# Optimization experiments

Hardware: AMD Instinct MI355X
Metric: run time of the kernel (lower is better)

The kernel has to match this reference:

```python
import jax, jax.numpy as jnp
import numpy as np

B, T, C = 512, 256, 384   # batch, seq (== block_size), n_embd
HS, BS = 64, 256          # head_size, block_size


def setup_inputs() -> dict:
    key = jax.random.key(0)
    ks = jax.random.split(key, 6)
    s = 1.0 / np.sqrt(C)
    s2 = 1.0 / np.sqrt(HS)
    return {
        "x": jax.random.normal(ks[0], (B, T, C), jnp.float32),
        "W_q": jax.random.normal(ks[1], (C, HS), jnp.float32) * s,
        "W_k": jax.random.normal(ks[2], (C, HS), jnp.float32) * s,
        "W_v": jax.random.normal(ks[3], (C, HS), jnp.float32) * s,
        "W_ql": jax.random.normal(ks[4], (HS, BS), jnp.float32) * s2,
        "W_kl": jax.random.normal(ks[5], (HS, BS), jnp.float32) * s2,
    }


def reference(x, W_q, W_k, W_v, W_ql, W_kl):
    # One head of self-attention, additive (tanh) score variant, eval mode.
    # x: [B,T,C]
    q = jnp.einsum("btc,ch->bth", x, W_q)          # [B,T,HS]
    k = jnp.einsum("btc,ch->bth", x, W_k)          # [B,T,HS]
    q_w = jnp.einsum("bth,hs->bts", q, W_ql)       # [B,T,BS]
    k_w = jnp.einsum("bth,hs->bts", k, W_kl)       # [B,T,BS]
    # NOTE: elementwise add (both [B,T,BS]) as in the torch code, then tanh.
    wei = jnp.tanh(q_w + k_w)                      # [B,T,T] since T == BS
    Tn = x.shape[1]
    causal = jnp.tril(jnp.ones((Tn, Tn), dtype=bool))
    wei = jnp.where(causal, wei, -jnp.inf)
    wei = jax.nn.softmax(wei, axis=-1)
    v = jnp.einsum("btc,ch->bth", x, W_v)          # [B,T,HS]
    out = jnp.einsum("bts,bsh->bth", wei, v)       # [B,T,HS]
    return out
```

## Files before the change

### kernel.cpp

```cpp
#include <hip/hip_runtime.h>

#define BATCH 512
#define TT    256
#define CC    384
#define HH    64

typedef float  f32x4 __attribute__((ext_vector_type(4)));
typedef short  s16x8 __attribute__((ext_vector_type(8)));

#define XS_OFF   0
#define WS_OFF   32768
#define VB_OFF   114688
#define SCR_OFF  147456
#define LDS_TOTAL 155648

__device__ __forceinline__ unsigned short f2bf(float f) {
    union { float f; unsigned u; } c; c.f = f;
    unsigned u = c.u;
    u += 0x7fffu + ((u >> 16) & 1u);
    return (unsigned short)(u >> 16);
}

__device__ __forceinline__ void gld_lds16(const void* g, void* l) {
    __builtin_amdgcn_global_load_lds(
        (const __attribute__((address_space(1))) unsigned int*)(unsigned long long)g,
        (__attribute__((address_space(3))) unsigned int*)(unsigned int)(unsigned long long)l,
        16, 0, 0);
}

__global__ void prep_w(const float* __restrict__ Wq, const float* __restrict__ Wk,
                       const float* __restrict__ Wv, const float* __restrict__ Wql,
                       const float* __restrict__ Wkl, unsigned short* __restrict__ wsW) {
    int gid = blockIdx.x * 256 + threadIdx.x;
    int k, n; float val;
    if (gid < CC * 256) {
        k = gid >> 8; int s = gid & 255; n = s;
        float acc = 0.f;
        for (int h = 0; h < HH; ++h)
            acc += Wq[k * HH + h] * Wql[h * 256 + s] + Wk[k * HH + h] * Wkl[h * 256 + s];
        val = acc;
    } else {
        int g2 = gid - CC * 256;
        k = g2 >> 6; int h = g2 & 63; n = 256 + h;
        val = Wv[k * HH + h];
    }
    int kc = k >> 6, kk = (k >> 5) & 1, ct = n >> 4;
    int lane = ((k >> 3) & 3) * 16 + (n & 15);
    int j = k & 7;
    wsW[((((kc * 2 + kk) * 20 + ct) * 64) + lane) * 8 + j] = f2bf(val);
}

__global__ __launch_bounds__(512, 2) void head_main(const float* __restrict__ x,
                                                    const unsigned short* __restrict__ wsW,
                                                    float* __restrict__ out) {
    extern __shared__ char sm[];
    unsigned short* Xs  = (unsigned short*)(sm + XS_OFF);
    unsigned short* Wsh = (unsigned short*)(sm + WS_OFF);
    unsigned short* Vb  = (unsigned short*)(sm + VB_OFF);

    const int b    = blockIdx.x;
    const int t    = threadIdx.x;
    const int w    = (t >> 6) & 7;
    const int lane = t & 63;
    const int q    = lane >> 4;
    const int cidx = lane & 15;
    const int rt0  = w;
    const int rt1  = 15 - w;
    unsigned short* scr = (unsigned short*)(sm + SCR_OFF) + w * 512;

    const float* xb = x + (size_t)b * (TT * CC);

    f32x4 accS0[8], accS1[16], accV[2][4];
#pragma unroll
    for (int i = 0; i < 8; ++i)  accS0[i] = (f32x4){0.f,0.f,0.f,0.f};
#pragma unroll
    for (int i = 0; i < 16; ++i) accS1[i] = (f32x4){0.f,0.f,0.f,0.f};
#pragma unroll
    for (int i = 0; i < 2; ++i)
#pragma unroll
        for (int j = 0; j < 4; ++j) accV[i][j] = (f32x4){0.f,0.f,0.f,0.f};

    int xrow[4], xkoff[4];
#pragma unroll
    for (int i = 0; i < 4; ++i) {
        int g = t + i * 512;
        int kk = g >> 10, rt = (g >> 6) & 15, L = g & 63;
        xrow[i]  = rt * 16 + (L & 15);
        xkoff[i] = kk * 32 + ((L >> 4) & 3) * 8;
    }

    float4 xf[8];
#pragma unroll
    for (int i = 0; i < 4; ++i) {
        const float4* p = (const float4*)(xb + xrow[i] * CC + xkoff[i]);
        xf[2*i]   = p[0];
        xf[2*i+1] = p[1];
    }
#pragma unroll
    for (int i = 0; i < 5; ++i) {
        int g = t + i * 512;
        gld_lds16(wsW + g * 8, Wsh + g * 8);
    }

    for (int kc = 0; kc < 6; ++kc) {
#pragma unroll
        for (int i = 0; i < 4; ++i) {
            int g = t + i * 512;
            float4 f0 = xf[2*i], f1 = xf[2*i+1];
            s16x8 v;
            v[0] = (short)f2bf(f0.x); v[1] = (short)f2bf(f0.y);
            v[2] = (short)f2bf(f0.z); v[3] = (short)f2bf(f0.w);
            v[4] = (short)f2bf(f1.x); v[5] = (short)f2bf(f1.y);
            v[6] = (short)f2bf(f1.z); v[7] = (short)f2bf(f1.w);
            *(s16x8*)(Xs + g * 8) = v;
        }
        __syncthreads();

        if (kc < 5) {
            const int kn = kc + 1;
#pragma unroll
            for (int i = 0; i < 4; ++i) {
                const float4* p = (const float4*)(xb + xrow[i] * CC + kn * 64 + xkoff[i]);
                xf[2*i]   = p[0];
                xf[2*i+1] = p[1];
            }
            const unsigned short* wsrc = wsW + (size_t)kn * 20480;
            unsigned short*       wdst = Wsh + (kn & 1) * 20480;
#pragma unroll
            for (int i = 0; i < 5; ++i) {
                int g = t + i * 512;
                gld_lds16(wsrc + g * 8, wdst + g * 8);
            }
        }

        const unsigned short* Wb = Wsh + (kc & 1) * 20480;
#pragma unroll
        for (int kk = 0; kk < 2; ++kk) {
            s16x8 a0 = *(const s16x8*)(Xs + ((kk * 16 + rt0) * 64 + lane) * 8);
            s16x8 a1 = *(const s16x8*)(Xs + ((kk * 16 + rt1) * 64 + lane) * 8);
#pragma unroll
            for (int ct = 0; ct < 16; ++ct) {
                if (ct <= rt1) {
                    s16x8 bf = *(const s16x8*)(Wb + ((kk * 20 + ct) * 64 + lane) * 8);
                    accS1[ct] = __builtin_amdgcn_mfma_f32_16x16x32_bf16(a1, bf, accS1[ct], 0, 0, 0);
                    if (ct < 8 && ct <= rt0)
                        accS0[ct] = __builtin_amdgcn_mfma_f32_16x16x32_bf16(a0, bf, accS0[ct], 0, 0, 0);
                }
            }
#pragma unroll
            for (int v2 = 0; v2 < 4; ++v2) {
                s16x8 bf = *(const s16x8*)(Wb + ((kk * 20 + 16 + v2) * 64 + lane) * 8);
                accV[0][v2] = __builtin_amdgcn_mfma_f32_16x16x32_bf16(a0, bf, accV[0][v2], 0, 0, 0);
                accV[1][v2] = __builtin_amdgcn_mfma_f32_16x16x32_bf16(a1, bf, accV[1][v2], 0, 0, 0);
            }
        }
        __syncthreads();
    }

    float rs0[4] = {0.f,0.f,0.f,0.f}, rs1[4] = {0.f,0.f,0.f,0.f};
    s16x8 pf0[4], pf1[8];

#pragma unroll
    for (int ch = 0; ch < 8; ++ch) {
        if (ch <= (rt1 >> 1)) {
#pragma unroll
            for (int sub = 0; sub < 2; ++sub) {
                const int ct = 2 * ch + sub;
                const int gcol = ct * 16 + cidx;
                const int c = sub * 16 + cidx;
#pragma unroll
                for (int rg = 0; rg < 4; ++rg) {
                    const int grow = rt1 * 16 + q * 4 + rg;
                    float e = 0.f;
                    if (ct <= rt1 && gcol <= grow) {
                        float sv = accS1[2 * ch + sub][rg];
                        float ex = __expf(2.f * sv);
                        float th = 1.f - __fdividef(2.f, ex + 1.f);
                        e = __expf(th);
                    }
                    rs1[rg] += e;
                    scr[((c >> 3) * 16 + q * 4 + rg) * 8 + (c & 7)] = f2bf(e);
                }
            }
            pf1[ch] = *(const s16x8*)(scr + lane * 8);
        }
    }
#pragma unroll
    for (int ch = 0; ch < 4; ++ch) {
        if (ch <= (rt0 >> 1)) {
#pragma unroll
            for (int sub = 0; sub < 2; ++sub) {
                const int ct = 2 * ch + sub;
                const int gcol = ct * 16 + cidx;
                const int c = sub * 16 + cidx;
#pragma unroll
                for (int rg = 0; rg < 4; ++rg) {
                    const int grow = rt0 * 16 + q * 4 + rg;
                    float e = 0.f;
                    if (ct <= rt0 && gcol <= grow) {
                        float sv = accS0[2 * ch + sub][rg];
                        float ex = __expf(2.f * sv);
                        float th = 1.f - __fdividef(2.f, ex + 1.f);
                        e = __expf(th);
                    }
                    rs0[rg] += e;
                    scr[((c >> 3) * 16 + q * 4 + rg) * 8 + (c & 7)] = f2bf(e);
                }
            }
            pf0[ch] = *(const s16x8*)(scr + lane * 8);
        }
    }

#pragma unroll
    for (int ri = 0; ri < 2; ++ri) {
        const int rt = ri ? rt1 : rt0;
#pragma unroll
        for (int vct = 0; vct < 4; ++vct)
#pragma unroll
            for (int rg = 0; rg < 4; ++rg) {
                int srow = rt * 16 + q * 4 + rg;
                Vb[((vct * 8 + (srow >> 5)) * 64 + ((srow >> 3) & 3) * 16 + cidx) * 8 + (srow & 7)] =
                    f2bf(accV[ri][vct][rg]);
            }
    }

#pragma unroll
    for (int rg = 0; rg < 4; ++rg) {
        float v0 = rs0[rg], v1 = rs1[rg];
        v0 += __shfl_xor(v0, 1); v0 += __shfl_xor(v0, 2);
        v0 += __shfl_xor(v0, 4); v0 += __shfl_xor(v0, 8);
        v1 += __shfl_xor(v1, 1); v1 += __shfl_xor(v1, 2);
        v1 += __shfl_xor(v1, 4); v1 += __shfl_xor(v1, 8);
        rs0[rg] = v0; rs1[rg] = v1;
    }

    __syncthreads();

    f32x4 acc2[2][4];
#pragma unroll
    for (int i = 0; i < 2; ++i)
#pragma unroll
        for (int j = 0; j < 4; ++j) acc2[i][j] = (f32x4){0.f,0.f,0.f,0.f};

    const int nch0 = rt0 >> 1, nch1 = rt1 >> 1;
#pragma unroll
    for (int ch = 0; ch < 8; ++ch) {
        if (ch <= nch1) {
            s16x8 vb[4];
#pragma unroll
            for (int vct = 0; vct < 4; ++vct)
                vb[vct] = *(const s16x8*)(Vb + ((vct * 8 + ch) * 64 + lane) * 8);
#pragma unroll
            for (int vct = 0; vct < 4; ++vct)
                acc2[1][vct] = __builtin_amdgcn_mfma_f32_16x16x32_bf16(pf1[ch], vb[vct], acc2[1][vct], 0, 0, 0);
            if (ch < 4 && ch <= nch0) {
#pragma unroll
                for (int vct = 0; vct < 4; ++vct)
                    acc2[0][vct] = __builtin_amdgcn_mfma_f32_16x16x32_bf16(pf0[ch], vb[vct], acc2[0][vct], 0, 0, 0);
            }
        }
    }

    float* ob = out + (size_t)b * (TT * HH);
#pragma unroll
    for (int ri = 0; ri < 2; ++ri) {
        const int rt = ri ? rt1 : rt0;
#pragma unroll
        for (int rg = 0; rg < 4; ++rg) {
            int row = rt * 16 + q * 4 + rg;
            float inv = __fdividef(1.f, ri ? rs1[rg] : rs0[rg]);
#pragma unroll
            for (int vct = 0; vct < 4; ++vct)
                ob[row * HH + vct * 16 + cidx] = acc2[ri][vct][rg] * inv;
        }
    }
}

extern "C" void kernel_launch(void* const* d_in, const int* in_sizes, int n_in,
                              void* d_out, int out_size, void* d_ws, size_t ws_size,
                              hipStream_t stream) {
    const float* x   = (const float*)d_in[0];
    const float* Wq  = (const float*)d_in[1];
    const float* Wk  = (const float*)d_in[2];
    const float* Wv  = (const float*)d_in[3];
    const float* Wql = (const float*)d_in[4];
    const float* Wkl = (const float*)d_in[5];
    unsigned short* wsW = (unsigned short*)d_ws;
    float* out = (float*)d_out;

    prep_w<<<480, 256, 0, stream>>>(Wq, Wk, Wv, Wql, Wkl, wsW);

    hipFuncSetAttribute((const void*)head_main,
                        hipFuncAttributeMaxDynamicSharedMemorySize, LDS_TOTAL);
    head_main<<<BATCH, 512, LDS_TOTAL, stream>>>(x, wsW, out);
}
```

Before: 320.4 us.

## Load X and weight fragments directly from global memory, dropping LDS staging

Each wave now loads the x rows it needs straight into registers, double-buffered across K chunks, and reads pre-swizzled bf16 weight fragments from global memory instead of staging both through LDS. This removes the per-chunk block barriers and shrinks LDS from about 152KB to 40KB, which could allow more resident blocks. In exchange, weight fragments are re-read from global/L2 by every wave, and register pressure rises from the doubled x buffers.

```diff
diff --git a/kernel.cpp b/kernel.cpp
--- a/kernel.cpp
+++ b/kernel.cpp
@@ -8,24 +8,15 @@
 typedef float  f32x4 __attribute__((ext_vector_type(4)));
 typedef short  s16x8 __attribute__((ext_vector_type(8)));
 
-#define XS_OFF   0
-#define WS_OFF   32768
-#define VB_OFF   114688
-#define SCR_OFF  147456
-#define LDS_TOTAL 155648
+#define VB_OFF   0
+#define SCR_OFF  32768
+#define LDS_TOTAL 40960
 
 __device__ __forceinline__ unsigned short f2bf(float f) {
     union { float f; unsigned u; } c; c.f = f;
     unsigned u = c.u;
     u += 0x7fffu + ((u >> 16) & 1u);
     return (unsigned short)(u >> 16);
-}
-
-__device__ __forceinline__ void gld_lds16(const void* g, void* l) {
-    __builtin_amdgcn_global_load_lds(
-        (const __attribute__((address_space(1))) unsigned int*)(unsigned long long)g,
-        (__attribute__((address_space(3))) unsigned int*)(unsigned int)(unsigned long long)l,
-        16, 0, 0);
 }
 
 __global__ void prep_w(const float* __restrict__ Wq, const float* __restrict__ Wk,
@@ -54,8 +45,6 @@
                                                     const unsigned short* __restrict__ wsW,
                                                     float* __restrict__ out) {
     extern __shared__ char sm[];
-    unsigned short* Xs  = (unsigned short*)(sm + XS_OFF);
-    unsigned short* Wsh = (unsigned short*)(sm + WS_OFF);
     unsigned short* Vb  = (unsigned short*)(sm + VB_OFF);
 
     const int b    = blockIdx.x;
@@ -70,6 +59,11 @@
 
     const float* xb = x + (size_t)b * (TT * CC);
 
+    const float* xa0 = xb + (rt0 * 16 + cidx) * CC + q * 8;
+    const float* xa1 = xb + (rt1 * 16 + cidx) * CC + q * 8;
+
+    const unsigned short* wlane = wsW + lane * 8;
+
     f32x4 accS0[8], accS1[16], accV[2][4];
 #pragma unroll
     for (int i = 0; i < 8; ++i)  accS0[i] = (f32x4){0.f,0.f,0.f,0.f};
@@ -80,68 +74,53 @@
 #pragma unroll
         for (int j = 0; j < 4; ++j) accV[i][j] = (f32x4){0.f,0.f,0.f,0.f};
 
-    int xrow[4], xkoff[4];
-#pragma unroll
-    for (int i = 0; i < 4; ++i) {
-        int g = t + i * 512;
-        int kk = g >> 10, rt = (g >> 6) & 15, L = g & 63;
-        xrow[i]  = rt * 16 + (L & 15);
-        xkoff[i] = kk * 32 + ((L >> 4) & 3) * 8;
-    }
-
-    float4 xf[8];
-#pragma unroll
-    for (int i = 0; i < 4; ++i) {
-        const float4* p = (const float4*)(xb + xrow[i] * CC + xkoff[i]);
-        xf[2*i]   = p[0];
-        xf[2*i+1] = p[1];
-    }
-#pragma unroll
-    for (int i = 0; i < 5; ++i) {
-        int g = t + i * 512;
-        gld_lds16(wsW + g * 8, Wsh + g * 8);
-    }
-
+    float4 xf[2][8];
+
+    auto loadX = [&](int s, int kcv) {
+#pragma unroll
+        for (int ri = 0; ri < 2; ++ri) {
+            const float* base = (ri ? xa1 : xa0) + kcv * 64;
+#pragma unroll
+            for (int kk = 0; kk < 2; ++kk) {
+                const float4* p = (const float4*)(base + kk * 32);
+                xf[s][ri * 4 + kk * 2]     = p[0];
+                xf[s][ri * 4 + kk * 2 + 1] = p[1];
+            }
+        }
+    };
+    auto pack8 = [&](const float4& f0, const float4& f1) -> s16x8 {
+        s16x8 v;
+        v[0] = (short)f2bf(f0.x); v[1] = (short)f2bf(f0.y);
+        v[2] = (short)f2bf(f0.z); v[3] = (short)f2bf(f0.w);
+        v[4] = (short)f2bf(f1.x); v[5] = (short)f2bf(f1.y);
+        v[6] = (short)f2bf(f1.z); v[7] = (short)f2bf(f1.w);
+        return v;
+    };
+
+    loadX(0, 0);
+
+#pragma unroll
     for (int kc = 0; kc < 6; ++kc) {
-#pragma unroll
-        for (int i = 0; i < 4; ++i) {
-            int g = t + i * 512;
-            float4 f0 = xf[2*i], f1 = xf[2*i+1];
-            s16x8 v;
-            v[0] = (short)f2bf(f0.x); v[1] = (short)f2bf(f0.y);
-            v[2] = (short)f2bf(f0.z); v[3] = (short)f2bf(f0.w);
-            v[4] = (short)f2bf(f1.x); v[5] = (short)f2bf(f1.y);
-            v[6] = (short)f2bf(f1.z); v[7] = (short)f2bf(f1.w);
-            *(s16x8*)(Xs + g * 8) = v;
-        }
-        __syncthreads();
-
-        if (kc < 5) {
-            const int kn = kc + 1;
-#pragma unroll
-            for (int i = 0; i < 4; ++i) {
-                const float4* p = (const float4*)(xb + xrow[i] * CC + kn * 64 + xkoff[i]);
-                xf[2*i]   = p[0];
-                xf[2*i+1] = p[1];
-            }
-            const unsigned short* wsrc = wsW + (size_t)kn * 20480;
-            unsigned short*       wdst = Wsh + (kn & 1) * 20480;
-#pragma unroll
-            for (int i = 0; i < 5; ++i) {
-                int g = t + i * 512;
-                gld_lds16(wsrc + g * 8, wdst + g * 8);
-            }
-        }
-
-        const unsigned short* Wb = Wsh + (kc & 1) * 20480;
+        if (kc < 5)
+            loadX((kc + 1) & 1, kc + 1);
+
+        s16x8 afr[2][2];
+#pragma unroll
+        for (int ri = 0; ri < 2; ++ri)
+#pragma unroll
+            for (int kk = 0; kk < 2; ++kk)
+                afr[ri][kk] = pack8(xf[kc & 1][ri * 4 + kk * 2], xf[kc & 1][ri * 4 + kk * 2 + 1]);
+
+        const unsigned short* wkc = wlane + (size_t)(kc * 2) * 20 * 512;
 #pragma unroll
         for (int kk = 0; kk < 2; ++kk) {
-            s16x8 a0 = *(const s16x8*)(Xs + ((kk * 16 + rt0) * 64 + lane) * 8);
-            s16x8 a1 = *(const s16x8*)(Xs + ((kk * 16 + rt1) * 64 + lane) * 8);
+            s16x8 a0 = afr[0][kk];
+            s16x8 a1 = afr[1][kk];
+            const unsigned short* wb = wkc + kk * (20 * 512);
 #pragma unroll
             for (int ct = 0; ct < 16; ++ct) {
                 if (ct <= rt1) {
-                    s16x8 bf = *(const s16x8*)(Wb + ((kk * 20 + ct) * 64 + lane) * 8);
+                    s16x8 bf = *(const s16x8*)(wb + ct * 512);
                     accS1[ct] = __builtin_amdgcn_mfma_f32_16x16x32_bf16(a1, bf, accS1[ct], 0, 0, 0);
                     if (ct < 8 && ct <= rt0)
                         accS0[ct] = __builtin_amdgcn_mfma_f32_16x16x32_bf16(a0, bf, accS0[ct], 0, 0, 0);
@@ -149,12 +128,11 @@
             }
 #pragma unroll
             for (int v2 = 0; v2 < 4; ++v2) {
-                s16x8 bf = *(const s16x8*)(Wb + ((kk * 20 + 16 + v2) * 64 + lane) * 8);
+                s16x8 bf = *(const s16x8*)(wb + (16 + v2) * 512);
                 accV[0][v2] = __builtin_amdgcn_mfma_f32_16x16x32_bf16(a0, bf, accV[0][v2], 0, 0, 0);
                 accV[1][v2] = __builtin_amdgcn_mfma_f32_16x16x32_bf16(a1, bf, accV[1][v2], 0, 0, 0);
             }
         }
-        __syncthreads();
     }
 
     float rs0[4] = {0.f,0.f,0.f,0.f}, rs1[4] = {0.f,0.f,0.f,0.f};
@@ -290,7 +268,5 @@
 
     prep_w<<<480, 256, 0, stream>>>(Wq, Wk, Wv, Wql, Wkl, wsW);
 
-    hipFuncSetAttribute((const void*)head_main,
-                        hipFuncAttributeMaxDynamicSharedMemorySize, LDS_TOTAL);
     head_main<<<BATCH, 512, LDS_TOTAL, stream>>>(x, wsW, out);
 }
```

Result: slower. 628.8 us (+96.3%).
